# Optimization experiments

Measured on AMD Instinct MI355X. Metric: run time of the kernel, lower is better.

## Reference

```python
import jax, jax.numpy as jnp
import numpy as np

M_IND = 1024   # inducing points
K_NN = 16      # nearest neighbors
JITTER = 1e-4


def rbf(X, Z):
    # unit-variance, unit-lengthscale RBF kernel; returns (K, squared distances)
    sq = jnp.sum(X * X, -1)[:, None] + jnp.sum(Z * Z, -1)[None, :] - 2.0 * (X @ Z.T)
    sq = jnp.maximum(sq, 0.0)
    return jnp.exp(-0.5 * sq), sq


def setup_inputs() -> dict:
    key = jax.random.key(0)
    k1, k2, k3 = jax.random.split(key, 3)
    return {
        "X": jax.random.normal(k1, (65536, 3), jnp.float32),
        "Z": jax.random.normal(k2, (M_IND, 3), jnp.float32),
        "Lu_raw": jax.random.normal(k3, (M_IND, M_IND), jnp.float32),
        "mu": jnp.zeros((M_IND,), jnp.float32),
    }


def reference(X, Z, Lu_raw, mu):
    N = X.shape[0]
    Kxx = jnp.ones((N,), X.dtype)                      # diag of RBF(X,X) is 1
    Kxz, dist = rbf(X, Z)                              # [N,M], [N,M]
    Kzz, _ = rbf(Z, Z)                                 # [M,M]

    # transform_to(lower_cholesky): strict lower triangle + exp(diag)
    Lu = jnp.tril(Lu_raw, -1) + jnp.diag(jnp.exp(jnp.diag(Lu_raw)))

    eyeM = jnp.eye(M_IND, dtype=X.dtype)
    L = jnp.linalg.cholesky(Kzz + JITTER * eyeM)       # [M,M]
    Kzz_j = L @ L.T                                    # == little_L @ little_L.T math (Kzz + jitter*I)
    Su = Lu @ Lu.T                                     # full variational covariance

    # K nearest inducing points per data point (argsort(dist)[:, :K])
    _, idx = jax.lax.top_k(-dist, K_NN)                # [N,K]

    lKzz = Kzz_j[idx[:, :, None], idx[:, None, :]]     # [N,K,K] gathered submatrices
    lS = Su[idx[:, :, None], idx[:, None, :]]          # [N,K,K]
    lKxz = jnp.take_along_axis(Kxz, idx, axis=1)       # [N,K]
    lmu = mu[idx]                                      # [N,K]

    eyeK = jnp.eye(K_NN, dtype=X.dtype)
    inv = jnp.linalg.inv(lKzz + JITTER * eyeK)         # batched tiny inverses [N,K,K]
    W = jnp.einsum('nk,nkj->nj', lKxz, inv)            # [N,K]

    mean = jnp.einsum('nk,nk->n', W, lmu)              # [N]
    cov = (Kxx
           - jnp.einsum('ni,nij,nj->n', W, lKzz, W)
           + jnp.einsum('ni,nij,nj->n', W, lS, W))
    std = jnp.sqrt(jnp.clip(cov, 0.05, None))          # qF scale = clamp(cov, 0.05)**0.5
    return jnp.stack([mean, std])                      # [2,N] qF parameters
```

## Files before the change

kernel.cpp:

```cpp
#include <hip/hip_runtime.h>
#include <math.h>

#define N_PTS 65536
#define M_IND 1024
#define KNN 16
#define JITTER 1e-4f

#define PACKED_FLOATS (M_IND * (M_IND + 1) / 2)
#define PACKED_BYTES  ((size_t)PACKED_FLOATS * sizeof(float))

#define TSU 32
#define SU_BLOCKS 528
#define PTS_PER_BLK 128
#define QSTRIDE 17
#define GRID_BLKS (N_PTS / PTS_PER_BLK)


__device__ __forceinline__ void su_tile(const float* __restrict__ Lu_raw,
                                        float* __restrict__ P,
                                        int bid, int tid,
                                        float (*As)[36], float (*Bs)[36]) {
    int rt = (int)((sqrtf(8.0f * (float)bid + 1.0f) - 1.0f) * 0.5f);
    while ((rt + 1) * (rt + 2) / 2 <= bid) ++rt;
    while (rt * (rt + 1) / 2 > bid) --rt;
    int ct = bid - rt * (rt + 1) / 2;
    int i0 = rt * TSU, j0 = ct * TSU;

    int tx = tid & 15, ty = tid >> 4;
    int sr = tid >> 3, sc = (tid & 7) << 2;
    float a00 = 0.f, a01 = 0.f, a10 = 0.f, a11 = 0.f;

    int nch = ct + 1;
    int gi = i0 + sr, gj = j0 + sr;
    float4 pa = *(const float4*)(Lu_raw + (unsigned)gi * M_IND + sc);
    float4 pb = *(const float4*)(Lu_raw + (unsigned)gj * M_IND + sc);

    for (int c = 0; c < nch; ++c) {
        int gk = (c << 5) + sc;
        float aa[4] = {pa.x, pa.y, pa.z, pa.w};
        float bb[4] = {pb.x, pb.y, pb.z, pb.w};
        #pragma unroll
        for (int q = 0; q < 4; ++q) {
            int k = gk + q;
            aa[q] = (k < gi) ? aa[q] : ((k == gi) ? __expf(aa[q]) : 0.0f);
            bb[q] = (k < gj) ? bb[q] : ((k == gj) ? __expf(bb[q]) : 0.0f);
        }
        *(float4*)&As[sr][sc] = make_float4(aa[0], aa[1], aa[2], aa[3]);
        *(float4*)&Bs[sr][sc] = make_float4(bb[0], bb[1], bb[2], bb[3]);
        __syncthreads();
        if (c + 1 < nch) {
            int kn = ((c + 1) << 5) + sc;
            pa = *(const float4*)(Lu_raw + (unsigned)gi * M_IND + kn);
            pb = *(const float4*)(Lu_raw + (unsigned)gj * M_IND + kn);
        }
        #pragma unroll
        for (int kk = 0; kk < 32; kk += 4) {
            float4 av0 = *(const float4*)&As[ty][kk];
            float4 av1 = *(const float4*)&As[ty + 16][kk];
            float4 bv0 = *(const float4*)&Bs[tx][kk];
            float4 bv1 = *(const float4*)&Bs[tx + 16][kk];
            a00 = fmaf(av0.x, bv0.x, fmaf(av0.y, bv0.y, fmaf(av0.z, bv0.z, fmaf(av0.w, bv0.w, a00))));
            a01 = fmaf(av0.x, bv1.x, fmaf(av0.y, bv1.y, fmaf(av0.z, bv1.z, fmaf(av0.w, bv1.w, a01))));
            a10 = fmaf(av1.x, bv0.x, fmaf(av1.y, bv0.y, fmaf(av1.z, bv0.z, fmaf(av1.w, bv0.w, a10))));
            a11 = fmaf(av1.x, bv1.x, fmaf(av1.y, bv1.y, fmaf(av1.z, bv1.z, fmaf(av1.w, bv1.w, a11))));
        }
        __syncthreads();
    }

    int ia = i0 + ty, ib = i0 + ty + 16;
    int ja = j0 + tx, jb = j0 + tx + 16;
    if (ja <= ia) P[((unsigned)ia * (ia + 1) >> 1) + ja] = a00;
    if (jb <= ia) P[((unsigned)ia * (ia + 1) >> 1) + jb] = a01;
    if (ja <= ib) P[((unsigned)ib * (ib + 1) >> 1) + ja] = a10;
    if (jb <= ib) P[((unsigned)ib * (ib + 1) >> 1) + jb] = a11;
}

__global__ __launch_bounds__(256) void su_kernel(const float* __restrict__ Lu_raw,
                                                 float* __restrict__ P) {
    __shared__ float As[TSU][36];
    __shared__ float Bs[TSU][36];
    su_tile(Lu_raw, P, blockIdx.x, threadIdx.x, As, Bs);
}

__device__ __forceinline__ void ce(unsigned long long& x, unsigned long long& y) {
    unsigned long long a = x, b = y;
    bool c = a < b;
    x = c ? a : b;
    y = c ? b : a;
}
__device__ __forceinline__ void ce(float& x, float& y) {
    float a = fminf(x, y), b = fmaxf(x, y);
    x = a; y = b;
}

template <typename KT>
__device__ __forceinline__ void sort16(KT* a) {
    #pragma unroll
    for (int p = 1; p < 16; p <<= 1)
        #pragma unroll
        for (int k = p; k >= 1; k >>= 1)
            #pragma unroll
            for (int j = k & (p - 1); j + k < 16; j += 2 * k)
                #pragma unroll
                for (int i = 0; i < k; ++i)
                    if (i + j + k < 16)
                        if (((i + j) / (2 * p)) == ((i + j + k) / (2 * p)))
                            ce(a[i + j], a[i + j + k]);
}

template <typename KT>
__device__ __forceinline__ void cleanup16(KT* a) {
    #pragma unroll
    for (int d = 8; d >= 1; d >>= 1)
        #pragma unroll
        for (int i = 0; i < 16; ++i)
            if ((i & d) == 0) ce(a[i], a[i | d]);
}

__device__ __forceinline__ float uval(float4 z, float xn0, float xn1, float xn2) {
    return fmaf(xn0, z.x, fmaf(xn1, z.y, fmaf(xn2, z.z, z.w)));
}

template <int MODE>
__global__ __launch_bounds__(256, 2) void vnngp_kernel(const float* __restrict__ X,
                                                       const float* __restrict__ Z,
                                                       const float* __restrict__ mu,
                                                       float* __restrict__ P,
                                                       const float* __restrict__ Lu_raw,
                                                       float* __restrict__ out) {
    __shared__ __align__(16) char smem[81408];
    float4* Zs = (float4*)smem;
    float* mus = (float*)(smem + 16384);
    unsigned long long* qb = (unsigned long long*)(smem + 20480);
    int tid = threadIdx.x;

    for (int r = tid; r < M_IND; r += 256) {
        float zx = Z[r * 3 + 0], zy = Z[r * 3 + 1], zz = Z[r * 3 + 2];
        Zs[r] = make_float4(zx, zy, zz, 0.5f * (zx * zx + zy * zy + zz * zz));
        mus[r] = mu[r];
    }
    __syncthreads();

    {
        int pt = tid >> 2, sub = tid & 3;
        int nA = blockIdx.x * PTS_PER_BLK + pt;
        int nB = nA + 64;
        float xA0 = X[nA * 3 + 0], xA1 = X[nA * 3 + 1], xA2 = X[nA * 3 + 2];
        float xB0 = X[nB * 3 + 0], xB1 = X[nB * 3 + 1], xB2 = X[nB * 3 + 2];
        float xqA = fmaf(xA0, xA0, fmaf(xA1, xA1, xA2 * xA2));
        float xqB = fmaf(xB0, xB0, fmaf(xB1, xB1, xB2 * xB2));
        float nA0 = -xA0, nA1 = -xA1, nA2 = -xA2;
        float nB0 = -xB0, nB1 = -xB1, nB2 = -xB2;
        int mbase = sub << 8;
        int rot = sub << 1;

        float TA[16], TB[16];
        #pragma unroll
        for (int j = 0; j < 16; ++j) { TA[j] = 3.4e38f; TB[j] = 3.4e38f; }
        #pragma unroll 1
        for (int c = 0; c < 16; ++c) {
            int base = mbase + (c << 4);
            #pragma unroll
            for (int j = 0; j < 16; ++j) {
                int m = base + ((j + rot) & 15);
                float4 z = Zs[m];
                TA[j] = fminf(TA[j], uval(z, nA0, nA1, nA2));
                TB[j] = fminf(TB[j], uval(z, nB0, nB1, nB2));
            }
        }
        sort16(TA);
        sort16(TB);
        #pragma unroll
        for (int round = 1; round <= 2; round <<= 1) {
            float oA[16], oB[16];
            #pragma unroll
            for (int i = 0; i < 16; ++i) {
                oA[i] = __shfl_xor(TA[i], round, 64);
                oB[i] = __shfl_xor(TB[i], round, 64);
            }
            #pragma unroll
            for (int i = 0; i < 16; ++i) {
                TA[i] = fminf(TA[i], oA[15 - i]);
                TB[i] = fminf(TB[i], oB[15 - i]);
            }
            cleanup16(TA);
            cleanup16(TB);
        }
        float TstarA = TA[15], TstarB = TB[15];

        unsigned short* mycA = ((unsigned short*)qb) + pt * (QSTRIDE * 4) + sub * 16;
        unsigned short* mycB = ((unsigned short*)qb) + (pt + 64) * (QSTRIDE * 4) + sub * 16;
        int cntA = 0, cntB = 0;
        #pragma unroll 1
        for (int c = 0; c < 16; ++c) {
            int base = mbase + (c << 4);
            #pragma unroll
            for (int j = 0; j < 16; ++j) {
                int m = base + ((j + rot) & 15);
                float4 z = Zs[m];
                float uA = uval(z, nA0, nA1, nA2);
                float uB = uval(z, nB0, nB1, nB2);
                if (uA <= TstarA) { if (cntA < 16) mycA[cntA] = (unsigned short)m; ++cntA; }
                if (uB <= TstarB) { if (cntB < 16) mycB[cntB] = (unsigned short)m; ++cntB; }
            }
        }

        int ovfA = cntA > 16 ? 1 : 0;
        ovfA |= __shfl_xor(ovfA, 1, 64);
        ovfA |= __shfl_xor(ovfA, 2, 64);
        int ovfB = cntB > 16 ? 1 : 0;
        ovfB |= __shfl_xor(ovfB, 1, 64);
        ovfB |= __shfl_xor(ovfB, 2, 64);

        if (!ovfA) {
            const unsigned long long* m64 = (const unsigned long long*)mycA;
            unsigned long long raw[4] = {m64[0], m64[1], m64[2], m64[3]};
            unsigned long long C[16];
            #pragma unroll
            for (int i = 0; i < 16; ++i) {
                int m = (int)((raw[i >> 2] >> ((i & 3) * 16)) & 0x3FF);
                float u = uval(Zs[m], nA0, nA1, nA2);
                float d = fmaxf(fmaf(2.0f, u, xqA), 0.0f);
                unsigned long long key =
                    ((unsigned long long)__float_as_uint(d) << 32) | (unsigned)m;
                C[i] = (i < cntA) ? key : ~0ULL;
            }
            sort16(C);
            #pragma unroll
            for (int round = 1; round <= 2; round <<= 1) {
                unsigned long long o[16];
                #pragma unroll
                for (int i = 0; i < 16; ++i) o[i] = __shfl_xor(C[i], round, 64);
                #pragma unroll
                for (int i = 0; i < 16; ++i) {
                    unsigned long long b = o[15 - i];
                    C[i] = C[i] < b ? C[i] : b;
                }
                cleanup16(C);
            }
            if (sub == 0) {
                #pragma unroll
                for (int i = 0; i < 16; ++i) qb[pt * QSTRIDE + i] = C[i];
            }
        } else if (sub == 0) {
            unsigned long long R[16];
            #pragma unroll
            for (int i = 0; i < 16; ++i) R[i] = ~0ULL;
            for (int m = 0; m < M_IND; ++m) {
                float u = uval(Zs[m], nA0, nA1, nA2);
                float d = fmaxf(fmaf(2.0f, u, xqA), 0.0f);
                unsigned long long kk =
                    ((unsigned long long)__float_as_uint(d) << 32) | (unsigned)m;
                if (kk < R[15]) {
                    #pragma unroll
                    for (int j = 0; j < 16; ++j) {
                        unsigned long long t = R[j];
                        bool cc = kk < t;
                        R[j] = cc ? kk : t;
                        kk = cc ? t : kk;
                    }
                }
            }
            #pragma unroll
            for (int i = 0; i < 16; ++i) qb[pt * QSTRIDE + i] = R[i];
        }

        if (!ovfB) {
            const unsigned long long* m64 = (const unsigned long long*)mycB;
            unsigned long long raw[4] = {m64[0], m64[1], m64[2], m64[3]};
            unsigned long long C[16];
            #pragma unroll
            for (int i = 0; i < 16; ++i) {
                int m = (int)((raw[i >> 2] >> ((i & 3) * 16)) & 0x3FF);
                float u = uval(Zs[m], nB0, nB1, nB2);
                float d = fmaxf(fmaf(2.0f, u, xqB), 0.0f);
                unsigned long long key =
                    ((unsigned long long)__float_as_uint(d) << 32) | (unsigned)m;
                C[i] = (i < cntB) ? key : ~0ULL;
            }
            sort16(C);
            #pragma unroll
            for (int round = 1; round <= 2; round <<= 1) {
                unsigned long long o[16];
                #pragma unroll
                for (int i = 0; i < 16; ++i) o[i] = __shfl_xor(C[i], round, 64);
                #pragma unroll
                for (int i = 0; i < 16; ++i) {
                    unsigned long long b = o[15 - i];
                    C[i] = C[i] < b ? C[i] : b;
                }
                cleanup16(C);
            }
            if (sub == 0) {
                #pragma unroll
                for (int i = 0; i < 16; ++i) qb[(pt + 64) * QSTRIDE + i] = C[i];
            }
        } else if (sub == 0) {
            unsigned long long R[16];
            #pragma unroll
            for (int i = 0; i < 16; ++i) R[i] = ~0ULL;
            for (int m = 0; m < M_IND; ++m) {
                float u = uval(Zs[m], nB0, nB1, nB2);
                float d = fmaxf(fmaf(2.0f, u, xqB), 0.0f);
                unsigned long long kk =
                    ((unsigned long long)__float_as_uint(d) << 32) | (unsigned)m;
                if (kk < R[15]) {
                    #pragma unroll
                    for (int j = 0; j < 16; ++j) {
                        unsigned long long t = R[j];
                        bool cc = kk < t;
                        R[j] = cc ? kk : t;
                        kk = cc ? t : kk;
                    }
                }
            }
            #pragma unroll
            for (int i = 0; i < 16; ++i) qb[(pt + 64) * QSTRIDE + i] = R[i];
        }
    }
    __syncthreads();

    int idx[KNN];
    float kv[KNN], musr[KNN];
    float nx[KNN], ny[KNN], nz[KNN], nq[KNN];
    if (tid < PTS_PER_BLK) {
        #pragma unroll
        for (int a = 0; a < KNN; ++a) {
            unsigned long long k = qb[tid * QSTRIDE + a];
            int ia = (int)(k & 0xFFFFFFFFULL);
            float d = __uint_as_float((unsigned)(k >> 32));
            idx[a] = ia;
            kv[a] = __expf(-0.5f * d);
            float4 z = Zs[ia];
            nx[a] = z.x; ny[a] = z.y; nz[a] = z.z; nq[a] = z.w;
            musr[a] = mus[ia];
        }
    }
    __syncthreads();
    if (tid >= PTS_PER_BLK) return;

    float* Ab = (float*)(smem + 11264) + tid * 137;

    #pragma unroll
    for (int r = 0; r < KNN; ++r) {
        Ab[r * (r + 1) / 2 + r] = 1.0f + 2.0f * JITTER;
        #pragma unroll
        for (int c = 0; c < r; ++c) {
            float dot = fmaf(nx[r], nx[c], fmaf(ny[r], ny[c], nz[r] * nz[c]));
            Ab[r * (r + 1) / 2 + c] = __expf(fminf(dot - nq[r] - nq[c], 0.0f));
        }
    }

    #pragma unroll
    for (int c = 0; c < KNN; ++c) {
        float diag = Ab[c * (c + 1) / 2 + c];
        #pragma unroll
        for (int k = 0; k < c; ++k) {
            float lv = Ab[c * (c + 1) / 2 + k];
            diag = fmaf(-lv, lv, diag);
        }
        float rinv = __frsqrt_rn(fmaxf(diag, 1e-12f));
        Ab[c * (c + 1) / 2 + c] = rinv;
        #pragma unroll
        for (int r = c + 1; r < KNN; ++r) {
            float v = Ab[r * (r + 1) / 2 + c];
            #pragma unroll
            for (int k = 0; k < c; ++k)
                v = fmaf(-Ab[r * (r + 1) / 2 + k], Ab[c * (c + 1) / 2 + k], v);
            Ab[r * (r + 1) / 2 + c] = v * rinv;
        }
    }

    float w[KNN];
    #pragma unroll
    for (int r = 0; r < KNN; ++r) {
        float v = kv[r];
        #pragma unroll
        for (int c = 0; c < r; ++c) v = fmaf(-Ab[r * (r + 1) / 2 + c], w[c], v);
        w[r] = v * Ab[r * (r + 1) / 2 + r];
    }
    #pragma unroll
    for (int r = KNN - 1; r >= 0; --r) {
        float v = w[r];
        #pragma unroll
        for (int c = r + 1; c < KNN; ++c) v = fmaf(-Ab[c * (c + 1) / 2 + r], w[c], v);
        w[r] = v * Ab[r * (r + 1) / 2 + r];
    }

    float wk = 0.f, ww = 0.f, mean = 0.f;
    #pragma unroll
    for (int a = 0; a < KNN; ++a) {
        wk = fmaf(w[a], kv[a], wk);
        ww = fmaf(w[a], w[a], ww);
        mean = fmaf(w[a], musr[a], mean);
    }

    float qs = 0.f;
    if (MODE != 0) {
        #pragma unroll
        for (int r = 0; r < KNN; ++r) {
            int a = idx[r];
            float wr = w[r];
            float rowacc = 0.f;
            #pragma unroll
            for (int c = 0; c < r; ++c) {
                int b = idx[c];
                int hi = a > b ? a : b;
                int lo = a > b ? b : a;
                rowacc = fmaf(w[c], P[((unsigned)hi * (hi + 1) >> 1) + lo], rowacc);
            }
            qs = fmaf(wr, fmaf(wr, P[((unsigned)a * (a + 1) >> 1) + a], 2.0f * rowacc), qs);
        }
    } else {
        int si[KNN]; float sw[KNN];
        #pragma unroll
        for (int a = 0; a < KNN; ++a) { si[a] = idx[a]; sw[a] = w[a]; }
        #pragma unroll
        for (int a = 1; a < KNN; ++a) {
            int iv = si[a]; float wv = sw[a];
            int b = a - 1;
            while (b >= 0 && si[b] > iv) { si[b + 1] = si[b]; sw[b + 1] = sw[b]; --b; }
            si[b + 1] = iv; sw[b + 1] = wv;
        }
        int s = 0;
        int kend = si[KNN - 1];
        for (int k = 0; k <= kend; ++k) {
            float v = 0.f;
            if (s < KNN && si[s] == k) {
                v = sw[s] * __expf(Lu_raw[(unsigned)k * M_IND + k]);
                ++s;
            }
            for (int a = s; a < KNN; ++a)
                v = fmaf(sw[a], Lu_raw[(unsigned)si[a] * M_IND + k], v);
            qs = fmaf(v, v, qs);
        }
    }

    int n = blockIdx.x * PTS_PER_BLK + tid;
    float cov = 1.0f - (wk - JITTER * ww) + qs;
    float sd = sqrtf(fmaxf(cov, 0.05f));
    out[n] = mean;
    out[N_PTS + n] = sd;
}

extern "C" void kernel_launch(void* const* d_in, const int* in_sizes, int n_in,
                              void* d_out, int out_size, void* d_ws, size_t ws_size,
                              hipStream_t stream) {
    const float* X      = (const float*)d_in[0];
    const float* Z      = (const float*)d_in[1];
    const float* Lu_raw = (const float*)d_in[2];
    const float* mu     = (const float*)d_in[3];
    float* out = (float*)d_out;

    if (ws_size >= PACKED_BYTES) {
        float* P = (float*)d_ws;
        su_kernel<<<SU_BLOCKS, 256, 0, stream>>>(Lu_raw, P);
        vnngp_kernel<1><<<GRID_BLKS, 256, 0, stream>>>(X, Z, mu, P, Lu_raw, out);
    } else {
        vnngp_kernel<0><<<GRID_BLKS, 256, 0, stream>>>(X, Z, mu, nullptr, Lu_raw, out);
    }
}
```

Measured before the change: 182.2 us.

## Fuse Su packed-tile computation into main kernel with grid-wide counter wait

Removes the separate su_kernel launch by having each of the 512 main-kernel blocks compute one or two packed Su tiles before the kNN phase, then signal an atomic counter. Blocks do the local Cholesky solve before spinning on the counter, so the wait overlaps with useful work. Shared memory shrinks so the Cholesky scratch reuses the start of the buffer. The cost is a memset launch and a spin-wait that relies on all blocks being co-resident or progressing. If the wait times out, the block silently drops the Su term, which would produce wrong results.

```diff
diff --git a/kernel.cpp b/kernel.cpp
--- a/kernel.cpp
+++ b/kernel.cpp
@@ -14,6 +14,7 @@
 #define PTS_PER_BLK 128
 #define QSTRIDE 17
 #define GRID_BLKS (N_PTS / PTS_PER_BLK)
+#define SPIN_MAX 32768
 
 
 __device__ __forceinline__ void su_tile(const float* __restrict__ Lu_raw,
@@ -127,11 +128,13 @@
                                                        const float* __restrict__ mu,
                                                        float* __restrict__ P,
                                                        const float* __restrict__ Lu_raw,
+                                                       unsigned int* __restrict__ ctr,
                                                        float* __restrict__ out) {
-    __shared__ __align__(16) char smem[81408];
+    __shared__ __align__(16) char smem[70160];
     float4* Zs = (float4*)smem;
     float* mus = (float*)(smem + 16384);
     unsigned long long* qb = (unsigned long long*)(smem + 20480);
+    int* flagp = (int*)(smem + 70144);
     int tid = threadIdx.x;
 
     for (int r = tid; r < M_IND; r += 256) {
@@ -139,7 +142,29 @@
         Zs[r] = make_float4(zx, zy, zz, 0.5f * (zx * zx + zy * zy + zz * zz));
         mus[r] = mu[r];
     }
-    __syncthreads();
+
+    if (MODE == 2) {
+        float (*As)[36] = (float (*)[36])(smem + 20480);
+        float (*Bs)[36] = (float (*)[36])(smem + 20480 + 4608);
+        int t = blockIdx.x;
+        #pragma unroll
+        for (int r = 16; r < 32; ++r) {
+            int s = (r * (r + 1)) >> 1;
+            if (t >= s) ++t;
+        }
+        su_tile(Lu_raw, P, t, tid, As, Bs);
+        if (blockIdx.x < 16) {
+            int r = 16 + blockIdx.x;
+            su_tile(Lu_raw, P, (r * (r + 1)) >> 1, tid, As, Bs);
+        }
+        __syncthreads();
+        if (tid == 0) {
+            __threadfence();
+            atomicAdd(ctr, 1u);
+        }
+    } else {
+        __syncthreads();
+    }
 
     {
         int pt = tid >> 2, sub = tid & 3;
@@ -337,66 +362,82 @@
         }
     }
     __syncthreads();
+
+    float* Ab = (float*)smem + tid * 137;
+    float w[KNN];
+    float wk = 0.f, ww = 0.f, mean = 0.f;
+    if (tid < PTS_PER_BLK) {
+        #pragma unroll
+        for (int r = 0; r < KNN; ++r) {
+            Ab[r * (r + 1) / 2 + r] = 1.0f + 2.0f * JITTER;
+            #pragma unroll
+            for (int c = 0; c < r; ++c) {
+                float dot = fmaf(nx[r], nx[c], fmaf(ny[r], ny[c], nz[r] * nz[c]));
+                Ab[r * (r + 1) / 2 + c] = __expf(fminf(dot - nq[r] - nq[c], 0.0f));
+            }
+        }
+
+        #pragma unroll
+        for (int c = 0; c < KNN; ++c) {
+            float diag = Ab[c * (c + 1) / 2 + c];
+            #pragma unroll
+            for (int k = 0; k < c; ++k) {
+                float lv = Ab[c * (c + 1) / 2 + k];
+                diag = fmaf(-lv, lv, diag);
+            }
+            float rinv = __frsqrt_rn(fmaxf(diag, 1e-12f));
+            Ab[c * (c + 1) / 2 + c] = rinv;
+            #pragma unroll
+            for (int r = c + 1; r < KNN; ++r) {
+                float v = Ab[r * (r + 1) / 2 + c];
+                #pragma unroll
+                for (int k = 0; k < c; ++k)
+                    v = fmaf(-Ab[r * (r + 1) / 2 + k], Ab[c * (c + 1) / 2 + k], v);
+                Ab[r * (r + 1) / 2 + c] = v * rinv;
+            }
+        }
+
+        #pragma unroll
+        for (int r = 0; r < KNN; ++r) {
+            float v = kv[r];
+            #pragma unroll
+            for (int c = 0; c < r; ++c) v = fmaf(-Ab[r * (r + 1) / 2 + c], w[c], v);
+            w[r] = v * Ab[r * (r + 1) / 2 + r];
+        }
+        #pragma unroll
+        for (int r = KNN - 1; r >= 0; --r) {
+            float v = w[r];
+            #pragma unroll
+            for (int c = r + 1; c < KNN; ++c) v = fmaf(-Ab[c * (c + 1) / 2 + r], w[c], v);
+            w[r] = v * Ab[r * (r + 1) / 2 + r];
+        }
+
+        #pragma unroll
+        for (int a = 0; a < KNN; ++a) {
+            wk = fmaf(w[a], kv[a], wk);
+            ww = fmaf(w[a], w[a], ww);
+            mean = fmaf(w[a], musr[a], mean);
+        }
+    }
+
+    bool havP = (MODE == 1);
+    if (MODE == 2) {
+        if (tid == 0) {
+            int ok = 1, iters = 0;
+            while (__hip_atomic_load(ctr, __ATOMIC_ACQUIRE, __HIP_MEMORY_SCOPE_AGENT)
+                   < (unsigned)GRID_BLKS) {
+                __builtin_amdgcn_s_sleep(8);
+                if (++iters > SPIN_MAX) { ok = 0; break; }
+            }
+            *flagp = ok;
+        }
+        __syncthreads();
+        havP = (*flagp != 0);
+    }
     if (tid >= PTS_PER_BLK) return;
 
-    float* Ab = (float*)(smem + 11264) + tid * 137;
-
-    #pragma unroll
-    for (int r = 0; r < KNN; ++r) {
-        Ab[r * (r + 1) / 2 + r] = 1.0f + 2.0f * JITTER;
-        #pragma unroll
-        for (int c = 0; c < r; ++c) {
-            float dot = fmaf(nx[r], nx[c], fmaf(ny[r], ny[c], nz[r] * nz[c]));
-            Ab[r * (r + 1) / 2 + c] = __expf(fminf(dot - nq[r] - nq[c], 0.0f));
-        }
-    }
-
-    #pragma unroll
-    for (int c = 0; c < KNN; ++c) {
-        float diag = Ab[c * (c + 1) / 2 + c];
-        #pragma unroll
-        for (int k = 0; k < c; ++k) {
-            float lv = Ab[c * (c + 1) / 2 + k];
-            diag = fmaf(-lv, lv, diag);
-        }
-        float rinv = __frsqrt_rn(fmaxf(diag, 1e-12f));
-        Ab[c * (c + 1) / 2 + c] = rinv;
-        #pragma unroll
-        for (int r = c + 1; r < KNN; ++r) {
-            float v = Ab[r * (r + 1) / 2 + c];
-            #pragma unroll
-            for (int k = 0; k < c; ++k)
-                v = fmaf(-Ab[r * (r + 1) / 2 + k], Ab[c * (c + 1) / 2 + k], v);
-            Ab[r * (r + 1) / 2 + c] = v * rinv;
-        }
-    }
-
-    float w[KNN];
-    #pragma unroll
-    for (int r = 0; r < KNN; ++r) {
-        float v = kv[r];
-        #pragma unroll
-        for (int c = 0; c < r; ++c) v = fmaf(-Ab[r * (r + 1) / 2 + c], w[c], v);
-        w[r] = v * Ab[r * (r + 1) / 2 + r];
-    }
-    #pragma unroll
-    for (int r = KNN - 1; r >= 0; --r) {
-        float v = w[r];
-        #pragma unroll
-        for (int c = r + 1; c < KNN; ++c) v = fmaf(-Ab[c * (c + 1) / 2 + r], w[c], v);
-        w[r] = v * Ab[r * (r + 1) / 2 + r];
-    }
-
-    float wk = 0.f, ww = 0.f, mean = 0.f;
-    #pragma unroll
-    for (int a = 0; a < KNN; ++a) {
-        wk = fmaf(w[a], kv[a], wk);
-        ww = fmaf(w[a], w[a], ww);
-        mean = fmaf(w[a], musr[a], mean);
-    }
-
     float qs = 0.f;
-    if (MODE != 0) {
+    if (MODE != 0 && havP) {
         #pragma unroll
         for (int r = 0; r < KNN; ++r) {
             int a = idx[r];
@@ -452,11 +493,16 @@
     const float* mu     = (const float*)d_in[3];
     float* out = (float*)d_out;
 
-    if (ws_size >= PACKED_BYTES) {
+    if (ws_size >= PACKED_BYTES + 64) {
+        float* P = (float*)d_ws;
+        unsigned int* ctr = (unsigned int*)((char*)d_ws + PACKED_BYTES);
+        hipMemsetAsync(ctr, 0, sizeof(unsigned int), stream);
+        vnngp_kernel<2><<<GRID_BLKS, 256, 0, stream>>>(X, Z, mu, P, Lu_raw, ctr, out);
+    } else if (ws_size >= PACKED_BYTES) {
         float* P = (float*)d_ws;
         su_kernel<<<SU_BLOCKS, 256, 0, stream>>>(Lu_raw, P);
-        vnngp_kernel<1><<<GRID_BLKS, 256, 0, stream>>>(X, Z, mu, P, Lu_raw, out);
+        vnngp_kernel<1><<<GRID_BLKS, 256, 0, stream>>>(X, Z, mu, P, Lu_raw, nullptr, out);
     } else {
-        vnngp_kernel<0><<<GRID_BLKS, 256, 0, stream>>>(X, Z, mu, nullptr, Lu_raw, out);
-    }
-}
+        vnngp_kernel<0><<<GRID_BLKS, 256, 0, stream>>>(X, Z, mu, nullptr, Lu_raw, nullptr, out);
+    }
+}
```

Measured after the change: 168.9 us. 1.08x faster.
